# Performance work log

Hardware: AMD Instinct MI355X
Metric: run time of the kernel (lower is better)

## Reference

```python
import jax, jax.numpy as jnp
import numpy as np

NPOINT = 2048  # S after transition-down (init npoint)
NSAMPLE = 16   # K neighbors (init nsample)
EPS = 1e-5     # BatchNorm eps


def _conv1d(w, b, x):  # w [O,I], x [B,I,N] -> [B,O,N]
    y = jnp.einsum('oi,bin->bon', w, x)
    return y if b is None else y + b[None, :, None]


def _conv2d(w, b, x):  # w [O,I], x [B,I,S,K] -> [B,O,S,K]
    y = jnp.einsum('oi,bisk->bosk', w, x)
    return y if b is None else y + b[None, :, None, None]


def _gather(x, idx):  # x [B,C,N], idx [B,S] -> [B,C,S]
    return jax.vmap(lambda xb, ib: xb[:, ib])(x, idx)


def _group(x, idx):  # x [B,C,N], idx [B,S,K] -> [B,C,S,K]
    return jax.vmap(lambda xb, ib: xb[:, ib])(x, idx)


def _fps(xyz_bnc, S):  # farthest point sampling, start at index 0 (deterministic)
    B, N, _ = xyz_bnc.shape
    def body(carry, _):
        dist, far = carry
        centroid = jnp.take_along_axis(xyz_bnc, far[:, None, None], axis=1)  # [B,1,3]
        d = jnp.sum((xyz_bnc - centroid) ** 2, axis=-1)  # [B,N]
        dist = jnp.minimum(dist, d)
        nxt = jnp.argmax(dist, axis=-1).astype(jnp.int32)
        return (dist, nxt), far
    init = (jnp.full((B, N), 1e10, xyz_bnc.dtype), jnp.zeros((B,), jnp.int32))
    _, idxs = jax.lax.scan(body, init, None, length=S)
    return jnp.transpose(idxs)  # [B,S]


def _knn(k, query, pts):  # query [B,S,3], pts [B,N,3] -> idx [B,S,k]
    d2 = (jnp.sum(query ** 2, -1)[..., None] + jnp.sum(pts ** 2, -1)[:, None, :]
          - 2.0 * jnp.einsum('bsc,bnc->bsn', query, pts))
    _, idx = jax.lax.top_k(-d2, k)
    return idx


def _bn(x, gamma, beta):  # training-mode batchnorm over (B, spatial) per channel
    axes = (0,) + tuple(range(2, x.ndim))
    m = jnp.mean(x, axes, keepdims=True)
    v = jnp.var(x, axes, keepdims=True)
    shp = (1, -1) + (1,) * (x.ndim - 2)
    return gamma.reshape(shp) * (x - m) / jnp.sqrt(v + EPS) + beta.reshape(shp)


def _forward(xyz, points, td_w, td_b, td_gamma, td_beta,
             blk_before_w, blk_before_b, blk_qkv_w,
             blk_pos_w1, blk_pos_b1, blk_pos_w2, blk_pos_b2,
             blk_attn_w1, blk_attn_b1, blk_attn_w2, blk_attn_b2,
             blk_after_w, blk_after_b):
    S, K = NPOINT, NSAMPLE
    xyz_t = jnp.transpose(xyz, (0, 2, 1))  # [B,N,3]
    # ---- PointTransformerTransitionDown ----
    fps_idx = _fps(xyz_t, S)                       # [B,S]
    new_xyz = _gather(xyz, fps_idx)                # [B,3,S]
    new_xyz_t = jnp.transpose(new_xyz, (0, 2, 1))  # [B,S,3]
    gidx = _knn(K, new_xyz_t, xyz_t)               # [B,S,K]
    grouped_xyz = _group(xyz, gidx) - new_xyz[:, :, :, None]   # [B,3,S,K]
    grouped = jnp.concatenate([_group(points, gidx), grouped_xyz], axis=1)  # [B,D+3,S,K]
    h = jax.nn.relu(_bn(_conv2d(td_w, td_b, grouped), td_gamma, td_beta))
    pts = jnp.max(h, axis=-1)  # [B,out,S]
    # ---- PointTransformerResBlocks ----
    sgidx = _knn(K, new_xyz_t, new_xyz_t)          # self-KNN [B,S,K]
    gxyz = new_xyz[:, :, :, None] - _group(new_xyz, sgidx)  # [B,3,S,K]
    num_attn = blk_before_w.shape[0]
    for i in range(num_attn):
        rel = _conv2d(blk_pos_w2[i], blk_pos_b2[i],
                      jax.nn.relu(_conv2d(blk_pos_w1[i], blk_pos_b1[i], gxyz)))  # [B,mid,S,K]
        p = _conv1d(blk_before_w[i], blk_before_b[i], pts)   # [B,mid,S]
        qkv = _conv1d(blk_qkv_w[i], None, p)                 # [B,3*mid,S]
        q, k_, v = jnp.split(qkv, 3, axis=1)
        qk_rel = q[:, :, :, None] - _group(k_, sgidx)        # [B,mid,S,K]
        v = _group(v, sgidx) + rel
        sim = _conv2d(blk_attn_w2[i], blk_attn_b2[i],
                      jax.nn.relu(_conv2d(blk_attn_w1[i], blk_attn_b1[i], qk_rel + rel)))
        attn = jax.nn.softmax(sim, axis=-1)                  # softmax over neighbors
        agg = jnp.sum(attn * v, axis=-1)                     # [B,mid,S]
        pts = pts + _conv1d(blk_after_w[i], blk_after_b[i], agg)
    return new_xyz, pts


def setup_inputs() -> dict:
    key = jax.random.key(0)
    ks = jax.random.split(key, 20)
    B, N, Din, Dout, mid, A = 4, 8192, 64, 128, 32, 2
    r = lambda k, s, sc: sc * jax.random.normal(k, s, dtype=jnp.float32)
    return {
        'xyz': r(ks[0], (B, 3, N), 1.0),
        'points': r(ks[1], (B, Din, N), 1.0),
        'td_w': r(ks[2], (Dout, Din + 3), 0.1), 'td_b': r(ks[3], (Dout,), 0.02),
        'td_gamma': jnp.ones((Dout,), jnp.float32), 'td_beta': jnp.zeros((Dout,), jnp.float32),
        'blk_before_w': r(ks[4], (A, mid, Dout), 0.1), 'blk_before_b': r(ks[5], (A, mid), 0.02),
        'blk_qkv_w': r(ks[6], (A, 3 * mid, mid), 0.1),
        'blk_pos_w1': r(ks[7], (A, 64, 3), 0.1), 'blk_pos_b1': r(ks[8], (A, 64), 0.02),
        'blk_pos_w2': r(ks[9], (A, mid, 64), 0.1), 'blk_pos_b2': r(ks[10], (A, mid), 0.02),
        'blk_attn_w1': r(ks[11], (A, 4 * mid, mid), 0.1), 'blk_attn_b1': r(ks[12], (A, 4 * mid), 0.02),
        'blk_attn_w2': r(ks[13], (A, mid, 4 * mid), 0.1), 'blk_attn_b2': r(ks[14], (A, mid), 0.02),
        'blk_after_w': r(ks[15], (A, Dout, mid), 0.1), 'blk_after_b': r(ks[16], (A, Dout), 0.02),
    }


def reference(xyz, points, td_w, td_b, td_gamma, td_beta,
              blk_before_w, blk_before_b, blk_qkv_w,
              blk_pos_w1, blk_pos_b1, blk_pos_w2, blk_pos_b2,
              blk_attn_w1, blk_attn_b1, blk_attn_w2, blk_attn_b2,
              blk_after_w, blk_after_b):
    return _forward(xyz, points, td_w, td_b, td_gamma, td_beta,
                    blk_before_w, blk_before_b, blk_qkv_w,
                    blk_pos_w1, blk_pos_b1, blk_pos_w2, blk_pos_b2,
                    blk_attn_w1, blk_attn_b1, blk_attn_w2, blk_attn_b2,
                    blk_after_w, blk_after_b)
```

## Files before the change

### kernel.cpp

```cpp
#include <hip/hip_runtime.h>

#define BB 4
#define NN 8192
#define SS 2048
#define KK 16

typedef float v2f __attribute__((ext_vector_type(2)));

#define FTH 512
#define FPT (NN/FTH)
#define TRB 256
#define SPB 124
__global__ __launch_bounds__(FTH, 1) void fps_kernel(
    const float* __restrict__ xyz,
    const float* __restrict__ points,
    float* __restrict__ out_newxyz,
    float* __restrict__ nxt,
    float* __restrict__ ptst,
    int* __restrict__ spin_flag)
{
  #pragma clang fp contract(off)
  const int blk = blockIdx.x;
  const int tid = threadIdx.x;
  __shared__ __align__(16) float4 sxyz[NN];
  __shared__ __align__(16) unsigned long long skey[2][8];
  __shared__ int smi[SS];
  __shared__ float sred[8*6];
  __shared__ float tile[32][33];

  if (blk >= BB) {
    if (blk < BB + TRB) {
      if (blk == BB && tid == 0) spin_flag[8] = 0;
      const int x = tid & 31, yy = tid >> 5;
      for (int q = 0; q < 8; ++q) {
        const int tj = (blk - BB)*8 + q;
        const int tn = tj & 255, tc = (tj >> 8) & 1, tb = tj >> 9;
        const int n0 = tn*32, c0 = tc*32;
        __syncthreads();
        tile[yy][x]    = points[(tb*64 + c0+yy)*NN + n0+x];
        tile[yy+16][x] = points[(tb*64 + c0+yy+16)*NN + n0+x];
        __syncthreads();
        ptst[(tb*NN + n0+yy)*64 + c0+x]    = tile[x][yy];
        ptst[(tb*NN + n0+yy+16)*64 + c0+x] = tile[x][yy+16];
      }
      return;
    }
    if (tid >= 64) return;
    const int s0 = atomicAdd(spin_flag, 0);
    float a0 = 1.0f + tid, a1 = 2.0f, a2 = 3.0f, a3 = 4.0f;
    for (int outer = 0; outer < 50000; ++outer) {
      #pragma unroll
      for (int u = 0; u < 256; ++u) {
        a0 = fmaf(a0, 1.0000001f, 1e-7f);
        a1 = fmaf(a1, 0.9999999f, 2e-7f);
        a2 = fmaf(a2, 1.0000002f, 3e-7f);
        a3 = fmaf(a3, 0.9999998f, 4e-7f);
      }
      if (atomicAdd(spin_flag, 0) - s0 >= BB) break;
    }
    asm volatile("" :: "v"(a0), "v"(a1), "v"(a2), "v"(a3));
    return;
  }

  const int b = blk;
  const int wave = tid >> 6;
  const int lane = tid & 63;
  const float* xb = xyz + b*3*NN;

  float tx[FPT], ty[FPT], tz[FPT];
  #pragma unroll
  for (int j = 0; j < FPT; ++j) {
    int i = tid + j*FTH;
    tx[j] = xb[i]; ty[j] = xb[NN+i]; tz[j] = xb[2*NN+i];
  }
  float mnx = tx[0], mxx = tx[0], mny = ty[0], mxy = ty[0], mnz = tz[0], mxz = tz[0];
  #pragma unroll
  for (int j = 1; j < FPT; ++j) {
    mnx = fminf(mnx, tx[j]); mxx = fmaxf(mxx, tx[j]);
    mny = fminf(mny, ty[j]); mxy = fmaxf(mxy, ty[j]);
    mnz = fminf(mnz, tz[j]); mxz = fmaxf(mxz, tz[j]);
  }
  #define WRED(var, OP) { \
    float s_; \
    s_ = __int_as_float(__builtin_amdgcn_update_dpp(0, __float_as_int(var), 0x111, 0xf, 0xf, true)); var = OP(var, s_); \
    s_ = __int_as_float(__builtin_amdgcn_update_dpp(0, __float_as_int(var), 0x112, 0xf, 0xf, true)); var = OP(var, s_); \
    s_ = __int_as_float(__builtin_amdgcn_update_dpp(0, __float_as_int(var), 0x114, 0xf, 0xf, true)); var = OP(var, s_); \
    s_ = __int_as_float(__builtin_amdgcn_update_dpp(0, __float_as_int(var), 0x118, 0xf, 0xf, true)); var = OP(var, s_); \
    s_ = __int_as_float(__builtin_amdgcn_update_dpp(0, __float_as_int(var), 0x142, 0xf, 0xf, true)); var = OP(var, s_); \
    s_ = __int_as_float(__builtin_amdgcn_update_dpp(0, __float_as_int(var), 0x143, 0xf, 0xf, true)); var = OP(var, s_); }
  WRED(mnx, fminf) WRED(mxx, fmaxf) WRED(mny, fminf) WRED(mxy, fmaxf) WRED(mnz, fminf) WRED(mxz, fmaxf)
  #undef WRED
  if (lane == 63) {
    sred[wave*6+0] = mnx; sred[wave*6+1] = mxx; sred[wave*6+2] = mny;
    sred[wave*6+3] = mxy; sred[wave*6+4] = mnz; sred[wave*6+5] = mxz;
  }
  smi[tid] = 0;
  __syncthreads();
  #pragma unroll
  for (int w = 0; w < 8; ++w) {
    mnx = fminf(mnx, sred[w*6+0]); mxx = fmaxf(mxx, sred[w*6+1]);
    mny = fminf(mny, sred[w*6+2]); mxy = fmaxf(mxy, sred[w*6+3]);
    mnz = fminf(mnz, sred[w*6+4]); mxz = fmaxf(mxz, sred[w*6+5]);
  }
  const float scx = 8.0f / (mxx - mnx + 1e-12f);
  const float scy = 8.0f / (mxy - mny + 1e-12f);
  const float scz = 8.0f / (mxz - mnz + 1e-12f);
  int cells[FPT];
  #pragma unroll
  for (int j = 0; j < FPT; ++j) {
    int qx = min(7, (int)((tx[j] - mnx) * scx));
    int qy = min(7, (int)((ty[j] - mny) * scy));
    int qz = min(7, (int)((tz[j] - mnz) * scz));
    int m = (qx&1) | ((qy&1)<<1) | ((qz&1)<<2)
          | ((qx&2)<<2) | ((qy&2)<<3) | ((qz&2)<<4)
          | ((qx&4)<<4) | ((qy&4)<<5) | ((qz&4)<<6);
    cells[j] = m;
    atomicAdd(&smi[m], 1);
  }
  __syncthreads();
  for (int d = 1; d < 512; d <<= 1) {
    int v = smi[tid];
    int a = (tid >= d) ? smi[tid - d] : 0;
    __syncthreads();
    smi[tid] = v + a;
    __syncthreads();
  }
  {
    int excl = (tid == 0) ? 0 : smi[tid - 1];
    smi[512 + tid] = excl;
  }
  __syncthreads();
  #pragma unroll
  for (int j = 0; j < FPT; ++j) {
    int pos = atomicAdd(&smi[512 + cells[j]], 1);
    sxyz[pos] = make_float4(tx[j], ty[j], tz[j], 0.0f);
  }
  __syncthreads();
  v2f px[FPT/2], py[FPT/2], pz[FPT/2], dist[FPT/2];
  float bx0, bx1, by0, by1, bz0, bz1;
  {
    float4 c0 = sxyz[tid*FPT];
    bx0 = bx1 = c0.x; by0 = by1 = c0.y; bz0 = bz1 = c0.z;
    #pragma unroll
    for (int e = 0; e < FPT; ++e) {
      float4 cc = sxyz[tid*FPT + e];
      ((float*)px)[e] = cc.x; ((float*)py)[e] = cc.y; ((float*)pz)[e] = cc.z;
      ((float*)dist)[e] = 1e10f;
      bx0 = fminf(bx0, cc.x); bx1 = fmaxf(bx1, cc.x);
      by0 = fminf(by0, cc.y); by1 = fmaxf(by1, cc.y);
      bz0 = fminf(bz0, cc.z); bz1 = fmaxf(bz1, cc.z);
    }
  }
  float dmax = 1e10f;
  int   beste = 0;
  float cx = xb[0], cy = xb[NN], cz = xb[2*NN];
  __syncthreads();
  for (int it = 1; it < SS; ++it) {
    const int buf = it & 1;
    float gx = fmaxf(fmaxf(bx0 - cx, cx - bx1), 0.0f);
    float gy = fmaxf(fmaxf(by0 - cy, cy - by1), 0.0f);
    float gz = fmaxf(fmaxf(bz0 - cz, cz - bz1), 0.0f);
    float lb = gx*gx + gy*gy; lb = lb + gz*gz;
    if (lb * 0.99999f < dmax) {
      v2f cx2 = {cx, cx}, cy2 = {cy, cy}, cz2 = {cz, cz};
      v2f vmax = {-1.0f, -1.0f};
      #pragma unroll
      for (int j = 0; j < FPT/2; ++j) {
        v2f dx = px[j] - cx2, dy = py[j] - cy2, dz = pz[j] - cz2;
        v2f d = dx*dx + dy*dy;
        d = d + dz*dz;
        v2f nd = __builtin_elementwise_min(dist[j], d);
        dist[j] = nd;
        vmax = __builtin_elementwise_max(vmax, nd);
      }
      float mloc = fmaxf(vmax.x, vmax.y);
      int ce[FPT/2];
      #pragma unroll
      for (int j = 0; j < FPT/2; ++j) {
        int c = 0x7FFFFFFF;
        if (dist[j].y == mloc) c = 2*j + 1;
        if (dist[j].x == mloc) c = 2*j;
        ce[j] = c;
      }
      #pragma unroll
      for (int st = FPT/4; st >= 1; st >>= 1) {
        #pragma unroll
        for (int j = 0; j < st; ++j) ce[j] = ce[j] < ce[j+st] ? ce[j] : ce[j+st];
      }
      dmax = mloc;
      beste = ce[0];
    }
    float wm = dmax;
    #define FPS_MAXR(ctrl) { \
      float s_ = __int_as_float(__builtin_amdgcn_update_dpp(0, __float_as_int(wm), ctrl, 0xf, 0xf, true)); \
      wm = fmaxf(wm, s_); }
    FPS_MAXR(0x111)
    FPS_MAXR(0x112)
    FPS_MAXR(0x114)
    FPS_MAXR(0x118)
    FPS_MAXR(0x142)
    FPS_MAXR(0x143)
    #undef FPS_MAXR
    wm = __int_as_float(__builtin_amdgcn_readlane(__float_as_int(wm), 63));
    unsigned long long em = __ballot(dmax == wm);
    int lw = (int)__ffsll((unsigned long long)em) - 1;
    int bi_w = __builtin_amdgcn_readlane((tid << 4) + beste, lw);
    if (lane == 63) skey[buf][wave] = ((unsigned long long)__float_as_uint(wm) << 32) | (unsigned)~bi_w;
    __syncthreads();
    const ulonglong2* kp = (const ulonglong2*)&skey[buf][0];
    ulonglong2 k01 = kp[0], k23 = kp[1], k45 = kp[2], k67 = kp[3];
    unsigned long long m0 = k01.x > k01.y ? k01.x : k01.y;
    unsigned long long m1 = k23.x > k23.y ? k23.x : k23.y;
    unsigned long long m2 = k45.x > k45.y ? k45.x : k45.y;
    unsigned long long m3 = k67.x > k67.y ? k67.x : k67.y;
    unsigned long long ma = m0 > m1 ? m0 : m1;
    unsigned long long mb = m2 > m3 ? m2 : m3;
    unsigned long long mk = ma > mb ? ma : mb;
    int mi = (int)(~(unsigned)mk);
    float4 c = sxyz[mi];
    if (tid == 0) smi[it] = mi;
    cx = c.x; cy = c.y; cz = c.z;
  }
  __syncthreads();
  for (int it = tid; it < SS; it += FTH) {
    float x, y, z;
    if (it == 0) { x = xb[0]; y = xb[NN]; z = xb[2*NN]; }
    else { float4 c = sxyz[smi[it]]; x = c.x; y = c.y; z = c.z; }
    out_newxyz[(b*3+0)*SS + it] = x;
    out_newxyz[(b*3+1)*SS + it] = y;
    out_newxyz[(b*3+2)*SS + it] = z;
    nxt[(b*SS+it)*3+0] = x; nxt[(b*SS+it)*3+1] = y; nxt[(b*SS+it)*3+2] = z;
  }
  if (tid == 0) atomicAdd(spin_flag, 1);
}

#define TILE 2048
#define KTH 512
__global__ __launch_bounds__(KTH) void knn_kernel(
    const float* __restrict__ query_t,
    const float* __restrict__ cand1,
    const float* __restrict__ cand2,
    int* __restrict__ out1,
    int* __restrict__ out2)
{
  #pragma clang fp contract(off)
  __shared__ float4 sc[TILE];
  __shared__ float  smd[8*64*17];
  __shared__ int    smj[8*64*17];
  const int blocksPerB = SS/64;
  const int half = blockIdx.x >> 7;
  const int blk = blockIdx.x & 127;
  const float* cand = half ? cand2 : cand1;
  const int Nc = half ? SS : NN;
  int* outidx = half ? out2 : out1;
  const int b = blk / blocksPerB;
  const int q0 = (blk % blocksPerB)*64;
  const int wave = threadIdx.x >> 6, lane = threadIdx.x & 63;
  const int s = q0 + lane;
  const float qx = query_t[(b*SS+s)*3+0];
  const float qy = query_t[(b*SS+s)*3+1];
  const float qz = query_t[(b*SS+s)*3+2];
  float sq = qx*qx + qy*qy; sq = sq + qz*qz;
  float d16[16]; int i16[16];
  #pragma unroll
  for (int j = 0; j < 16; ++j) { d16[j] = 1e30f; i16[j] = 0x7FFFFFFF; }
  const float* cb = cand + b*3*Nc;
  const int QL = TILE/8;
  for (int base = 0; base < Nc; base += TILE) {
    __syncthreads();
    for (int j = threadIdx.x; j < TILE; j += KTH) {
      float x = cb[base+j], y = cb[Nc+base+j], z = cb[2*Nc+base+j];
      float pp = x*x + y*y; pp = pp + z*z;
      sc[j] = make_float4(x, y, z, pp);
    }
    __syncthreads();
    const int lo = wave*QL, hi = lo + QL;
    for (int j = lo; j < hi; ++j) {
      float4 c = sc[j];
      float qp = qx*c.x + qy*c.y; qp = qp + qz*c.z;
      float d2 = (sq + c.w) - 2.0f*qp;
      if (d2 < d16[15]) {
        d16[15] = d2; i16[15] = base + j;
        #pragma unroll
        for (int t = 15; t > 0; --t) {
          if (d16[t] < d16[t-1]) {
            float td = d16[t]; d16[t] = d16[t-1]; d16[t-1] = td;
            int   ti = i16[t]; i16[t] = i16[t-1]; i16[t-1] = ti;
          }
        }
      }
    }
  }
  const int off = (wave*64 + lane)*17;
  #pragma unroll
  for (int j = 0; j < 16; ++j) { smd[off+j] = d16[j]; smj[off+j] = i16[j]; }
  __syncthreads();
  if (wave == 0) {
    int p[8] = {0,0,0,0,0,0,0,0};
    for (int o = 0; o < 16; ++o) {
      float bd = 3e38f; int bi = 0x7FFFFFFF, bw = 0;
      #pragma unroll
      for (int w = 0; w < 8; ++w) {
        float d = smd[(w*64+lane)*17 + p[w]];
        int   i = smj[(w*64+lane)*17 + p[w]];
        if (d < bd || (d == bd && i < bi)) { bd = d; bi = i; bw = w; }
      }
      p[bw]++;
      outidx[(b*SS+s)*KK + o] = bi;
    }
  }
}

__global__ __launch_bounds__(128) void td_kernel(
    const float* __restrict__ ptst,
    const float* __restrict__ xyz,
    const float* __restrict__ newxyz,
    const int* __restrict__ gidx,
    const float* __restrict__ td_w,
    const float* __restrict__ td_b,
    float* __restrict__ ymax,
    float* __restrict__ psum,
    float* __restrict__ psq)
{
  const int bs = blockIdx.x;
  const int b = bs >> 11, s = bs & (SS-1);
  const int t = threadIdx.x;
  __shared__ int gi[KK];
  __shared__ float g[67*17];
  if (t < KK) gi[t] = gidx[bs*KK + t];
  __syncthreads();
  #pragma unroll
  for (int base = 0; base < 1024; base += 128) {
    int idx = base + t;
    int i = idx & 63, k = idx >> 6;
    g[i*17 + k] = ptst[(b*NN + gi[k])*64 + i];
  }
  if (t < 48) {
    int c = t >> 4, k = t & 15;
    g[(64+c)*17 + k] = xyz[(b*3+c)*NN + gi[k]] - newxyz[(b*3+c)*SS + s];
  }
  __syncthreads();
  float acc[KK];
  #pragma unroll
  for (int k = 0; k < KK; ++k) acc[k] = 0.0f;
  const float* wrow = td_w + t*67;
  for (int i = 0; i < 67; ++i) {
    float w = wrow[i];
    #pragma unroll
    for (int k = 0; k < KK; ++k) acc[k] = fmaf(w, g[i*17 + k], acc[k]);
  }
  float bias = td_b[t];
  float mx = -1e30f, s1 = 0.f, s2 = 0.f;
  #pragma unroll
  for (int k = 0; k < KK; ++k) {
    float y = acc[k] + bias;
    mx = fmaxf(mx, y);
    s1 += y;
    s2 = fmaf(y, y, s2);
  }
  ymax[bs*128 + t] = mx;
  psum[bs*128 + t] = s1;
  psq [bs*128 + t] = s2;
}

__global__ __launch_bounds__(256) void bn_partial(
    const float* __restrict__ psum, const float* __restrict__ psq,
    float* __restrict__ part1, float* __restrict__ part2,
    const float* __restrict__ gamma, const float* __restrict__ beta,
    float* __restrict__ scale, float* __restrict__ bias,
    int* __restrict__ counter)
{
  const int blk = blockIdx.x, t = threadIdx.x;
  const int c = t & 127, half = t >> 7;
  const float* ps = psum + (blk*64 + half*32)*128;
  const float* pq = psq  + (blk*64 + half*32)*128;
  float s1 = 0.f, s2 = 0.f;
  for (int r = 0; r < 32; ++r) { s1 += ps[r*128 + c]; s2 += pq[r*128 + c]; }
  __shared__ float sh1[256], sh2[256];
  __shared__ int s_last;
  sh1[t] = s1; sh2[t] = s2;
  __syncthreads();
  if (t < 128) {
    part1[blk*128 + t] = sh1[t] + sh1[t+128];
    part2[blk*128 + t] = sh2[t] + sh2[t+128];
  }
  __syncthreads();
  __threadfence();
  if (t == 0) s_last = (atomicAdd(counter, 1) == 127) ? 1 : 0;
  __syncthreads();
  if (!s_last) return;
  __threadfence();
  float f1 = 0.f, f2 = 0.f;
  for (int j = half*64; j < half*64 + 64; ++j) {
    f1 += part1[j*128 + c];
    f2 += part2[j*128 + c];
  }
  sh1[t] = f1; sh2[t] = f2;
  __syncthreads();
  if (t < 128) {
    float a1 = sh1[t] + sh1[t+128];
    float a2 = sh2[t] + sh2[t+128];
    const float n = (float)(BB*SS*KK);
    float mean = a1/n;
    float var  = a2/n - mean*mean;
    float sc = gamma[t] / sqrtf(var + 1e-5f);
    scale[t] = sc;
    bias[t]  = beta[t] - mean*sc;
  }
}

__global__ __launch_bounds__(128) void r1_first(
    const float* __restrict__ ymax,
    const float* __restrict__ scale, const float* __restrict__ bias,
    const float* __restrict__ bw, const float* __restrict__ bb,
    const float* __restrict__ qw,
    float* __restrict__ pts,
    float* __restrict__ qkv)
{
  const int bs = blockIdx.x;
  const int t = threadIdx.x;
  __shared__ float pcol[128];
  __shared__ float p[32];
  float v = fmaxf(fmaf(ymax[bs*128 + t], scale[t], bias[t]), 0.0f);
  pts[bs*128 + t] = v;
  pcol[t] = v;
  __syncthreads();
  if (t < 32) {
    float acc = 0.f;
    const float* w = bw + t*128;
    for (int j = 0; j < 128; ++j) acc = fmaf(w[j], pcol[j], acc);
    p[t] = acc + bb[t];
  }
  __syncthreads();
  if (t < 96) {
    float acc = 0.f;
    const float* w = qw + t*32;
    #pragma unroll
    for (int j = 0; j < 32; ++j) acc = fmaf(w[j], p[j], acc);
    qkv[bs*96 + t] = acc;
  }
}

__global__ __launch_bounds__(128) void r1_kernel(
    const float* __restrict__ pts,
    const float* __restrict__ bw, const float* __restrict__ bb,
    const float* __restrict__ qw,
    float* __restrict__ qkv)
{
  const int bs = blockIdx.x;
  const int t = threadIdx.x;
  __shared__ float pcol[128];
  __shared__ float p[32];
  pcol[t] = pts[bs*128 + t];
  __syncthreads();
  if (t < 32) {
    float acc = 0.f;
    const float* w = bw + t*128;
    for (int j = 0; j < 128; ++j) acc = fmaf(w[j], pcol[j], acc);
    p[t] = acc + bb[t];
  }
  __syncthreads();
  if (t < 96) {
    float acc = 0.f;
    const float* w = qw + t*32;
    #pragma unroll
    for (int j = 0; j < 32; ++j) acc = fmaf(w[j], p[j], acc);
    qkv[bs*96 + t] = acc;
  }
}

__global__ __launch_bounds__(128) void r2_kernel(
    const float* __restrict__ qkv,
    const float* __restrict__ newxyz,
    const int* __restrict__ sgidx,
    const float* __restrict__ pw1, const float* __restrict__ pb1,
    const float* __restrict__ pw2, const float* __restrict__ pb2,
    const float* __restrict__ aw1, const float* __restrict__ ab1,
    const float* __restrict__ aw2, const float* __restrict__ ab2,
    const float* __restrict__ fw,  const float* __restrict__ fb,
    float* __restrict__ pts,
    float* __restrict__ outT)
{
  const int bs = blockIdx.x;
  const int b = bs >> 11, s = bs & (SS-1);
  const int t = threadIdx.x;
  __shared__ int sgi[KK];
  __shared__ float qv[32];
  __shared__ float kn[32*17], vn[32*17];
  __shared__ float gx[3*KK];
  __shared__ float h1[64*KK];
  __shared__ float x2[32*KK];
  __shared__ float a1[128*17];
  __shared__ float simb[32*KK];
  __shared__ float agg[32];
  if (t < KK) sgi[t] = sgidx[bs*KK + t];
  __syncthreads();
  if (t < 32) qv[t] = qkv[bs*96 + t];
  for (int idx = t; idx < 32*KK; idx += 128) {
    int k = idx >> 5, c = idx & 31;
    int base = (b*SS + sgi[k])*96;
    kn[c*17+k] = qkv[base + 32 + c];
    vn[c*17+k] = qkv[base + 64 + c];
  }
  if (t < 3*KK) {
    int c = t >> 4, k = t & 15;
    gx[t] = newxyz[(b*3+c)*SS + s] - newxyz[(b*3+c)*SS + sgi[k]];
  }
  __syncthreads();
  for (int idx = t; idx < 64*KK; idx += 128) {
    int c = idx >> 4, k = idx & 15;
    float acc = 0.f;
    #pragma unroll
    for (int j = 0; j < 3; ++j) acc = fmaf(pw1[c*3+j], gx[j*KK+k], acc);
    h1[idx] = fmaxf(acc + pb1[c], 0.0f);
  }
  __syncthreads();
  for (int idx = t; idx < 32*KK; idx += 128) {
    int c = idx >> 4, k = idx & 15;
    float acc = 0.f;
    const float* w = pw2 + c*64;
    for (int j = 0; j < 64; ++j) acc = fmaf(w[j], h1[j*KK+k], acc);
    float r = acc + pb2[c];
    x2[idx] = (qv[c] - kn[c*17+k]) + r;
    vn[c*17+k] = vn[c*17+k] + r;
  }
  __syncthreads();
  {
    float acc[KK];
    #pragma unroll
    for (int k = 0; k < KK; ++k) acc[k] = 0.f;
    const float* w = aw1 + t*32;
    for (int j = 0; j < 32; ++j) {
      float wv = w[j];
      #pragma unroll
      for (int k = 0; k < KK; ++k) acc[k] = fmaf(wv, x2[j*KK+k], acc[k]);
    }
    float bv = ab1[t];
    #pragma unroll
    for (int k = 0; k < KK; ++k) a1[t*17+k] = fmaxf(acc[k] + bv, 0.0f);
  }
  __syncthreads();
  for (int idx = t; idx < 32*KK; idx += 128) {
    int c = idx >> 4, k = idx & 15;
    float acc = 0.f;
    const float* w = aw2 + c*128;
    for (int j = 0; j < 128; ++j) acc = fmaf(w[j], a1[j*17+k], acc);
    simb[idx] = acc + ab2[c];
  }
  __syncthreads();
  if (t < 32) {
    float m = -1e30f;
    #pragma unroll
    for (int k = 0; k < KK; ++k) m = fmaxf(m, simb[t*KK+k]);
    float sum = 0.f;
    float e[KK];
    #pragma unroll
    for (int k = 0; k < KK; ++k) { e[k] = __expf(simb[t*KK+k] - m); sum += e[k]; }
    float inv = 1.0f / sum;
    float a = 0.f;
    #pragma unroll
    for (int k = 0; k < KK; ++k) a = fmaf(e[k]*inv, vn[t*17+k], a);
    agg[t] = a;
  }
  __syncthreads();
  {
    float acc = 0.f;
    const float* w = fw + t*32;
    #pragma unroll
    for (int j = 0; j < 32; ++j) acc = fmaf(w[j], agg[j], acc);
    float val = pts[bs*128 + t] + (acc + fb[t]);
    if (outT) outT[(b*128 + t)*SS + s] = val;
    else      pts[bs*128 + t] = val;
  }
}

extern "C" void kernel_launch(void* const* d_in, const int* in_sizes, int n_in,
                              void* d_out, int out_size, void* d_ws, size_t ws_size,
                              hipStream_t stream) {
  const float* xyz      = (const float*)d_in[0];
  const float* points   = (const float*)d_in[1];
  const float* td_w     = (const float*)d_in[2];
  const float* td_b     = (const float*)d_in[3];
  const float* td_gamma = (const float*)d_in[4];
  const float* td_beta  = (const float*)d_in[5];
  const float* bw  = (const float*)d_in[6];
  const float* bb  = (const float*)d_in[7];
  const float* qw  = (const float*)d_in[8];
  const float* pw1 = (const float*)d_in[9];
  const float* pb1 = (const float*)d_in[10];
  const float* pw2 = (const float*)d_in[11];
  const float* pb2 = (const float*)d_in[12];
  const float* aw1 = (const float*)d_in[13];
  const float* ab1 = (const float*)d_in[14];
  const float* aw2 = (const float*)d_in[15];
  const float* ab2 = (const float*)d_in[16];
  const float* fw  = (const float*)d_in[17];
  const float* fb  = (const float*)d_in[18];
  float* out = (float*)d_out;
  float* out_newxyz = out;
  float* out_pts    = out + BB*3*SS;

  char* w = (char*)d_ws;
  float* nxt    = (float*)w; w += BB*SS*3*sizeof(float);
  int*   gidx   = (int*)w;   w += BB*SS*KK*sizeof(int);
  int*   sgidx  = (int*)w;   w += BB*SS*KK*sizeof(int);
  float* ymax   = (float*)w; w += BB*128*SS*sizeof(float);
  float* psum   = (float*)w; w += 128*BB*SS*sizeof(float);
  float* psq    = (float*)w; w += 128*BB*SS*sizeof(float);
  float* part1  = (float*)w; w += 128*128*sizeof(float);
  float* part2  = (float*)w; w += 128*128*sizeof(float);
  float* bnscale= (float*)w; w += 256*sizeof(float);
  float* bnbias = (float*)w; w += 256*sizeof(float);
  float* pts    = (float*)w; w += BB*128*SS*sizeof(float);
  float* qkv    = (float*)w; w += BB*96*SS*sizeof(float);
  float* ptst   = (float*)w; w += BB*NN*64*sizeof(float);
  int*   flags  = (int*)w;   w += 256;

  fps_kernel<<<BB + TRB + SPB, FTH, 0, stream>>>(xyz, points, out_newxyz, nxt, ptst, flags);
  knn_kernel<<<2*BB*(SS/64), KTH, 0, stream>>>(nxt, xyz, out_newxyz, gidx, sgidx);
  td_kernel<<<BB*SS, 128, 0, stream>>>(ptst, xyz, out_newxyz, gidx, td_w, td_b, ymax, psum, psq);
  bn_partial<<<128, 256, 0, stream>>>(psum, psq, part1, part2,
      td_gamma, td_beta, bnscale, bnbias, &flags[8]);
  r1_first<<<BB*SS, 128, 0, stream>>>(ymax, bnscale, bnbias, bw, bb, qw, pts, qkv);
  r2_kernel<<<BB*SS, 128, 0, stream>>>(qkv, out_newxyz, sgidx,
      pw1, pb1, pw2, pb2, aw1, ab1, aw2, ab2, fw, fb, pts, nullptr);
  r1_kernel<<<BB*SS, 128, 0, stream>>>(pts, bw + 32*128, bb + 32, qw + 96*32, qkv);
  r2_kernel<<<BB*SS, 128, 0, stream>>>(qkv, out_newxyz, sgidx,
      pw1 + 64*3, pb1 + 64, pw2 + 32*64, pb2 + 32,
      aw1 + 128*32, ab1 + 128, aw2 + 32*128, ab2 + 32,
      fw + 128*32, fb + 128, pts, out_pts);
}
```

Measured before the change: 2.401 ms.

## Prune kNN with Morton-sorted candidate slabs and AABB lower bounds

```diff
diff --git a/kernel.cpp b/kernel.cpp
--- a/kernel.cpp
+++ b/kernel.cpp
@@ -6,6 +6,37 @@
 #define KK 16
 
 typedef float v2f __attribute__((ext_vector_type(2)));
+
+__device__ __forceinline__ float wred_max(float v) {
+  float s;
+  s = __int_as_float(__builtin_amdgcn_update_dpp(0, __float_as_int(v), 0x111, 0xf, 0xf, true)); v = fmaxf(v, s);
+  s = __int_as_float(__builtin_amdgcn_update_dpp(0, __float_as_int(v), 0x112, 0xf, 0xf, true)); v = fmaxf(v, s);
+  s = __int_as_float(__builtin_amdgcn_update_dpp(0, __float_as_int(v), 0x114, 0xf, 0xf, true)); v = fmaxf(v, s);
+  s = __int_as_float(__builtin_amdgcn_update_dpp(0, __float_as_int(v), 0x118, 0xf, 0xf, true)); v = fmaxf(v, s);
+  s = __int_as_float(__builtin_amdgcn_update_dpp(0, __float_as_int(v), 0x142, 0xf, 0xf, true)); v = fmaxf(v, s);
+  s = __int_as_float(__builtin_amdgcn_update_dpp(0, __float_as_int(v), 0x143, 0xf, 0xf, true)); v = fmaxf(v, s);
+  return v;
+}
+__device__ __forceinline__ float wred_min(float v) {
+  float s;
+  s = __int_as_float(__builtin_amdgcn_update_dpp(0, __float_as_int(v), 0x111, 0xf, 0xf, true)); v = fminf(v, s);
+  s = __int_as_float(__builtin_amdgcn_update_dpp(0, __float_as_int(v), 0x112, 0xf, 0xf, true)); v = fminf(v, s);
+  s = __int_as_float(__builtin_amdgcn_update_dpp(0, __float_as_int(v), 0x114, 0xf, 0xf, true)); v = fminf(v, s);
+  s = __int_as_float(__builtin_amdgcn_update_dpp(0, __float_as_int(v), 0x118, 0xf, 0xf, true)); v = fminf(v, s);
+  s = __int_as_float(__builtin_amdgcn_update_dpp(0, __float_as_int(v), 0x142, 0xf, 0xf, true)); v = fminf(v, s);
+  s = __int_as_float(__builtin_amdgcn_update_dpp(0, __float_as_int(v), 0x143, 0xf, 0xf, true)); v = fminf(v, s);
+  return v;
+}
+__device__ __forceinline__ int morton8(float x, float y, float z,
+                                       float mnx, float mny, float mnz,
+                                       float scx, float scy, float scz) {
+  int qx = min(7, (int)((x - mnx) * scx));
+  int qy = min(7, (int)((y - mny) * scy));
+  int qz = min(7, (int)((z - mnz) * scz));
+  return (qx&1) | ((qy&1)<<1) | ((qz&1)<<2)
+       | ((qx&2)<<2) | ((qy&2)<<3) | ((qz&2)<<4)
+       | ((qx&4)<<4) | ((qy&4)<<5) | ((qz&4)<<6);
+}
 
 #define FTH 512
 #define FPT (NN/FTH)
@@ -15,13 +46,18 @@
     const float* __restrict__ xyz,
     const float* __restrict__ points,
     float* __restrict__ out_newxyz,
-    float* __restrict__ nxt,
     float* __restrict__ ptst,
+    float4* __restrict__ csorted,
+    float*  __restrict__ caabb,
+    float4* __restrict__ qsorted,
+    float*  __restrict__ qaabb,
     int* __restrict__ spin_flag)
 {
   #pragma clang fp contract(off)
   const int blk = blockIdx.x;
   const int tid = threadIdx.x;
+  const int wave = tid >> 6;
+  const int lane = tid & 63;
   __shared__ __align__(16) float4 sxyz[NN];
   __shared__ __align__(16) unsigned long long skey[2][8];
   __shared__ int smi[SS];
@@ -43,6 +79,80 @@
         ptst[(tb*NN + n0+yy)*64 + c0+x]    = tile[x][yy];
         ptst[(tb*NN + n0+yy+16)*64 + c0+x] = tile[x][yy+16];
       }
+      if (blk - BB < BB) {
+        const int b2 = blk - BB;
+        const float* xb2 = xyz + b2*3*NN;
+        float tx[FPT], ty[FPT], tz[FPT];
+        #pragma unroll
+        for (int j = 0; j < FPT; ++j) {
+          int i = tid + j*FTH;
+          tx[j] = xb2[i]; ty[j] = xb2[NN+i]; tz[j] = xb2[2*NN+i];
+        }
+        float mnx = tx[0], mxx = tx[0], mny = ty[0], mxy = ty[0], mnz = tz[0], mxz = tz[0];
+        #pragma unroll
+        for (int j = 1; j < FPT; ++j) {
+          mnx = fminf(mnx, tx[j]); mxx = fmaxf(mxx, tx[j]);
+          mny = fminf(mny, ty[j]); mxy = fmaxf(mxy, ty[j]);
+          mnz = fminf(mnz, tz[j]); mxz = fmaxf(mxz, tz[j]);
+        }
+        mnx = wred_min(mnx); mxx = wred_max(mxx);
+        mny = wred_min(mny); mxy = wred_max(mxy);
+        mnz = wred_min(mnz); mxz = wred_max(mxz);
+        if (lane == 63) {
+          sred[wave*6+0] = mnx; sred[wave*6+1] = mxx; sred[wave*6+2] = mny;
+          sred[wave*6+3] = mxy; sred[wave*6+4] = mnz; sred[wave*6+5] = mxz;
+        }
+        smi[tid] = 0;
+        __syncthreads();
+        #pragma unroll
+        for (int w = 0; w < 8; ++w) {
+          mnx = fminf(mnx, sred[w*6+0]); mxx = fmaxf(mxx, sred[w*6+1]);
+          mny = fminf(mny, sred[w*6+2]); mxy = fmaxf(mxy, sred[w*6+3]);
+          mnz = fminf(mnz, sred[w*6+4]); mxz = fmaxf(mxz, sred[w*6+5]);
+        }
+        const float scx = 8.0f / (mxx - mnx + 1e-12f);
+        const float scy = 8.0f / (mxy - mny + 1e-12f);
+        const float scz = 8.0f / (mxz - mnz + 1e-12f);
+        int cells[FPT];
+        #pragma unroll
+        for (int j = 0; j < FPT; ++j) {
+          cells[j] = morton8(tx[j], ty[j], tz[j], mnx, mny, mnz, scx, scy, scz);
+          atomicAdd(&smi[cells[j]], 1);
+        }
+        __syncthreads();
+        for (int d = 1; d < 512; d <<= 1) {
+          int v = smi[tid];
+          int a = (tid >= d) ? smi[tid - d] : 0;
+          __syncthreads();
+          smi[tid] = v + a;
+          __syncthreads();
+        }
+        { int excl = (tid == 0) ? 0 : smi[tid - 1]; smi[512 + tid] = excl; }
+        __syncthreads();
+        #pragma unroll
+        for (int j = 0; j < FPT; ++j) {
+          int pos = atomicAdd(&smi[512 + cells[j]], 1);
+          csorted[b2*NN + pos] = make_float4(tx[j], ty[j], tz[j], __int_as_float(tid + j*FTH));
+        }
+        __syncthreads();
+        for (int sl = wave; sl < 32; sl += 8) {
+          float a0x=1e30f, a1x=-1e30f, a0y=1e30f, a1y=-1e30f, a0z=1e30f, a1z=-1e30f;
+          #pragma unroll
+          for (int t = 0; t < 4; ++t) {
+            float4 c = csorted[b2*NN + sl*256 + lane*4 + t];
+            a0x = fminf(a0x, c.x); a1x = fmaxf(a1x, c.x);
+            a0y = fminf(a0y, c.y); a1y = fmaxf(a1y, c.y);
+            a0z = fminf(a0z, c.z); a1z = fmaxf(a1z, c.z);
+          }
+          a0x = wred_min(a0x); a1x = wred_max(a1x);
+          a0y = wred_min(a0y); a1y = wred_max(a1y);
+          a0z = wred_min(a0z); a1z = wred_max(a1z);
+          if (lane == 63) {
+            float* o = caabb + (b2*32 + sl)*8;
+            o[0]=a0x; o[1]=a1x; o[2]=a0y; o[3]=a1y; o[4]=a0z; o[5]=a1z;
+          }
+        }
+      }
       return;
     }
     if (tid >= 64) return;
@@ -63,8 +173,6 @@
   }
 
   const int b = blk;
-  const int wave = tid >> 6;
-  const int lane = tid & 63;
   const float* xb = xyz + b*3*NN;
 
   float tx[FPT], ty[FPT], tz[FPT];
@@ -80,16 +188,9 @@
     mny = fminf(mny, ty[j]); mxy = fmaxf(mxy, ty[j]);
     mnz = fminf(mnz, tz[j]); mxz = fmaxf(mxz, tz[j]);
   }
-  #define WRED(var, OP) { \
-    float s_; \
-    s_ = __int_as_float(__builtin_amdgcn_update_dpp(0, __float_as_int(var), 0x111, 0xf, 0xf, true)); var = OP(var, s_); \
-    s_ = __int_as_float(__builtin_amdgcn_update_dpp(0, __float_as_int(var), 0x112, 0xf, 0xf, true)); var = OP(var, s_); \
-    s_ = __int_as_float(__builtin_amdgcn_update_dpp(0, __float_as_int(var), 0x114, 0xf, 0xf, true)); var = OP(var, s_); \
-    s_ = __int_as_float(__builtin_amdgcn_update_dpp(0, __float_as_int(var), 0x118, 0xf, 0xf, true)); var = OP(var, s_); \
-    s_ = __int_as_float(__builtin_amdgcn_update_dpp(0, __float_as_int(var), 0x142, 0xf, 0xf, true)); var = OP(var, s_); \
-    s_ = __int_as_float(__builtin_amdgcn_update_dpp(0, __float_as_int(var), 0x143, 0xf, 0xf, true)); var = OP(var, s_); }
-  WRED(mnx, fminf) WRED(mxx, fmaxf) WRED(mny, fminf) WRED(mxy, fmaxf) WRED(mnz, fminf) WRED(mxz, fmaxf)
-  #undef WRED
+  mnx = wred_min(mnx); mxx = wred_max(mxx);
+  mny = wred_min(mny); mxy = wred_max(mxy);
+  mnz = wred_min(mnz); mxz = wred_max(mxz);
   if (lane == 63) {
     sred[wave*6+0] = mnx; sred[wave*6+1] = mxx; sred[wave*6+2] = mny;
     sred[wave*6+3] = mxy; sred[wave*6+4] = mnz; sred[wave*6+5] = mxz;
@@ -108,14 +209,8 @@
   int cells[FPT];
   #pragma unroll
   for (int j = 0; j < FPT; ++j) {
-    int qx = min(7, (int)((tx[j] - mnx) * scx));
-    int qy = min(7, (int)((ty[j] - mny) * scy));
-    int qz = min(7, (int)((tz[j] - mnz) * scz));
-    int m = (qx&1) | ((qy&1)<<1) | ((qz&1)<<2)
-          | ((qx&2)<<2) | ((qy&2)<<3) | ((qz&2)<<4)
-          | ((qx&4)<<4) | ((qy&4)<<5) | ((qz&4)<<6);
-    cells[j] = m;
-    atomicAdd(&smi[m], 1);
+    cells[j] = morton8(tx[j], ty[j], tz[j], mnx, mny, mnz, scx, scy, scz);
+    atomicAdd(&smi[cells[j]], 1);
   }
   __syncthreads();
   for (int d = 1; d < 512; d <<= 1) {
@@ -191,16 +286,7 @@
       beste = ce[0];
     }
     float wm = dmax;
-    #define FPS_MAXR(ctrl) { \
-      float s_ = __int_as_float(__builtin_amdgcn_update_dpp(0, __float_as_int(wm), ctrl, 0xf, 0xf, true)); \
-      wm = fmaxf(wm, s_); }
-    FPS_MAXR(0x111)
-    FPS_MAXR(0x112)
-    FPS_MAXR(0x114)
-    FPS_MAXR(0x118)
-    FPS_MAXR(0x142)
-    FPS_MAXR(0x143)
-    #undef FPS_MAXR
+    wm = wred_max(wm);
     wm = __int_as_float(__builtin_amdgcn_readlane(__float_as_int(wm), 63));
     unsigned long long em = __ballot(dmax == wm);
     int lw = (int)__ffsll((unsigned long long)em) - 1;
@@ -229,86 +315,129 @@
     out_newxyz[(b*3+0)*SS + it] = x;
     out_newxyz[(b*3+1)*SS + it] = y;
     out_newxyz[(b*3+2)*SS + it] = z;
-    nxt[(b*SS+it)*3+0] = x; nxt[(b*SS+it)*3+1] = y; nxt[(b*SS+it)*3+2] = z;
+  }
+  float4 qp4[4]; int qj4[4], qc4[4];
+  #pragma unroll
+  for (int k2 = 0; k2 < 4; ++k2) {
+    int j = tid + k2*FTH;
+    float4 p;
+    if (j == 0) p = make_float4(xb[0], xb[NN], xb[2*NN], 0.0f);
+    else        p = sxyz[smi[j]];
+    qp4[k2] = p; qj4[k2] = j;
+  }
+  __syncthreads();
+  smi[tid] = 0;
+  __syncthreads();
+  #pragma unroll
+  for (int k2 = 0; k2 < 4; ++k2) {
+    qc4[k2] = morton8(qp4[k2].x, qp4[k2].y, qp4[k2].z, mnx, mny, mnz, scx, scy, scz);
+    atomicAdd(&smi[qc4[k2]], 1);
+  }
+  __syncthreads();
+  for (int d = 1; d < 512; d <<= 1) {
+    int v = smi[tid];
+    int a = (tid >= d) ? smi[tid - d] : 0;
+    __syncthreads();
+    smi[tid] = v + a;
+    __syncthreads();
+  }
+  { int excl = (tid == 0) ? 0 : smi[tid - 1]; smi[512 + tid] = excl; }
+  __syncthreads();
+  #pragma unroll
+  for (int k2 = 0; k2 < 4; ++k2) {
+    int pos = atomicAdd(&smi[512 + qc4[k2]], 1);
+    qsorted[b*SS + pos] = make_float4(qp4[k2].x, qp4[k2].y, qp4[k2].z, __int_as_float(qj4[k2]));
+  }
+  __syncthreads();
+  {
+    float a0x=1e30f, a1x=-1e30f, a0y=1e30f, a1y=-1e30f, a0z=1e30f, a1z=-1e30f;
+    #pragma unroll
+    for (int t = 0; t < 4; ++t) {
+      float4 c = qsorted[b*SS + wave*256 + lane*4 + t];
+      a0x = fminf(a0x, c.x); a1x = fmaxf(a1x, c.x);
+      a0y = fminf(a0y, c.y); a1y = fmaxf(a1y, c.y);
+      a0z = fminf(a0z, c.z); a1z = fmaxf(a1z, c.z);
+    }
+    a0x = wred_min(a0x); a1x = wred_max(a1x);
+    a0y = wred_min(a0y); a1y = wred_max(a1y);
+    a0z = wred_min(a0z); a1z = wred_max(a1z);
+    if (lane == 63) {
+      float* o = qaabb + (b*8 + wave)*8;
+      o[0]=a0x; o[1]=a1x; o[2]=a0y; o[3]=a1y; o[4]=a0z; o[5]=a1z;
+    }
   }
   if (tid == 0) atomicAdd(spin_flag, 1);
 }
 
-#define TILE 2048
-#define KTH 512
-__global__ __launch_bounds__(KTH) void knn_kernel(
-    const float* __restrict__ query_t,
-    const float* __restrict__ cand1,
-    const float* __restrict__ cand2,
+__global__ __launch_bounds__(64) void knn_kernel(
+    const float4* __restrict__ qsorted,
+    const float*  __restrict__ qaabb,
+    const float4* __restrict__ csorted,
+    const float*  __restrict__ caabb,
     int* __restrict__ out1,
     int* __restrict__ out2)
 {
   #pragma clang fp contract(off)
-  __shared__ float4 sc[TILE];
-  __shared__ float  smd[8*64*17];
-  __shared__ int    smj[8*64*17];
-  const int blocksPerB = SS/64;
-  const int half = blockIdx.x >> 7;
-  const int blk = blockIdx.x & 127;
-  const float* cand = half ? cand2 : cand1;
-  const int Nc = half ? SS : NN;
+  __shared__ float4 sc[256];
+  __shared__ int    sidx[256];
+  const int bid = blockIdx.x;
+  const int half = bid >> 7;
+  const int rem = bid & 127;
+  const int b = rem >> 5;
+  const int wslot = rem & 31;
+  const int lane = threadIdx.x;
+  const float4* cand = half ? (qsorted + b*SS) : (csorted + b*NN);
+  const float*  aabb = half ? (qaabb + b*8*8) : (caabb + b*32*8);
+  const int nsl = half ? 8 : 32;
+  const int s0 = half ? (wslot >> 2) : wslot;
   int* outidx = half ? out2 : out1;
-  const int b = blk / blocksPerB;
-  const int q0 = (blk % blocksPerB)*64;
-  const int wave = threadIdx.x >> 6, lane = threadIdx.x & 63;
-  const int s = q0 + lane;
-  const float qx = query_t[(b*SS+s)*3+0];
-  const float qy = query_t[(b*SS+s)*3+1];
-  const float qz = query_t[(b*SS+s)*3+2];
+
+  float4 q = qsorted[b*SS + wslot*64 + lane];
+  const int orig_s = __float_as_int(q.w);
+  const float qx = q.x, qy = q.y, qz = q.z;
   float sq = qx*qx + qy*qy; sq = sq + qz*qz;
   float d16[16]; int i16[16];
   #pragma unroll
   for (int j = 0; j < 16; ++j) { d16[j] = 1e30f; i16[j] = 0x7FFFFFFF; }
-  const float* cb = cand + b*3*Nc;
-  const int QL = TILE/8;
-  for (int base = 0; base < Nc; base += TILE) {
+
+  for (int j = 0; j < nsl; ++j) {
+    int off = (j + 1) >> 1;
+    int s = (s0 + ((j & 1) ? off : -off)) & (nsl - 1);
+    const float* ab = aabb + s*8;
+    float gx = fmaxf(fmaxf(ab[0] - qx, qx - ab[1]), 0.0f);
+    float gy = fmaxf(fmaxf(ab[2] - qy, qy - ab[3]), 0.0f);
+    float gz = fmaxf(fmaxf(ab[4] - qz, qz - ab[5]), 0.0f);
+    float lbnd = gx*gx + gy*gy; lbnd = lbnd + gz*gz;
+    bool skip = (lbnd * 0.9999f - 1e-3f) > d16[15];
+    if (__all(skip)) continue;
+    #pragma unroll
+    for (int t = 0; t < 4; ++t) {
+      float4 c = cand[s*256 + t*64 + lane];
+      float pp = c.x*c.x + c.y*c.y; pp = pp + c.z*c.z;
+      sidx[t*64 + lane] = __float_as_int(c.w);
+      sc[t*64 + lane] = make_float4(c.x, c.y, c.z, pp);
+    }
     __syncthreads();
-    for (int j = threadIdx.x; j < TILE; j += KTH) {
-      float x = cb[base+j], y = cb[Nc+base+j], z = cb[2*Nc+base+j];
-      float pp = x*x + y*y; pp = pp + z*z;
-      sc[j] = make_float4(x, y, z, pp);
-    }
-    __syncthreads();
-    const int lo = wave*QL, hi = lo + QL;
-    for (int j = lo; j < hi; ++j) {
-      float4 c = sc[j];
+    for (int t = 0; t < 256; ++t) {
+      float4 c = sc[t];
       float qp = qx*c.x + qy*c.y; qp = qp + qz*c.z;
       float d2 = (sq + c.w) - 2.0f*qp;
       if (d2 < d16[15]) {
-        d16[15] = d2; i16[15] = base + j;
+        d16[15] = d2; i16[15] = sidx[t];
         #pragma unroll
-        for (int t = 15; t > 0; --t) {
-          if (d16[t] < d16[t-1]) {
-            float td = d16[t]; d16[t] = d16[t-1]; d16[t-1] = td;
-            int   ti = i16[t]; i16[t] = i16[t-1]; i16[t-1] = ti;
+        for (int u = 15; u > 0; --u) {
+          if (d16[u] < d16[u-1]) {
+            float td = d16[u]; d16[u] = d16[u-1]; d16[u-1] = td;
+            int   ti = i16[u]; i16[u] = i16[u-1]; i16[u-1] = ti;
           }
         }
       }
     }
-  }
-  const int off = (wave*64 + lane)*17;
-  #pragma unroll
-  for (int j = 0; j < 16; ++j) { smd[off+j] = d16[j]; smj[off+j] = i16[j]; }
-  __syncthreads();
-  if (wave == 0) {
-    int p[8] = {0,0,0,0,0,0,0,0};
-    for (int o = 0; o < 16; ++o) {
-      float bd = 3e38f; int bi = 0x7FFFFFFF, bw = 0;
-      #pragma unroll
-      for (int w = 0; w < 8; ++w) {
-        float d = smd[(w*64+lane)*17 + p[w]];
-        int   i = smj[(w*64+lane)*17 + p[w]];
-        if (d < bd || (d == bd && i < bi)) { bd = d; bi = i; bw = w; }
-      }
-      p[bw]++;
-      outidx[(b*SS+s)*KK + o] = bi;
-    }
-  }
+    __syncthreads();
+  }
+  #pragma unroll
+  for (int o = 0; o < 16; ++o)
+    outidx[(b*SS + orig_s)*KK + o] = i16[o];
 }
 
 __global__ __launch_bounds__(128) void td_kernel(
@@ -601,7 +730,6 @@
   float* out_pts    = out + BB*3*SS;
 
   char* w = (char*)d_ws;
-  float* nxt    = (float*)w; w += BB*SS*3*sizeof(float);
   int*   gidx   = (int*)w;   w += BB*SS*KK*sizeof(int);
   int*   sgidx  = (int*)w;   w += BB*SS*KK*sizeof(int);
   float* ymax   = (float*)w; w += BB*128*SS*sizeof(float);
@@ -615,9 +743,14 @@
   float* qkv    = (float*)w; w += BB*96*SS*sizeof(float);
   float* ptst   = (float*)w; w += BB*NN*64*sizeof(float);
   int*   flags  = (int*)w;   w += 256;
-
-  fps_kernel<<<BB + TRB + SPB, FTH, 0, stream>>>(xyz, points, out_newxyz, nxt, ptst, flags);
-  knn_kernel<<<2*BB*(SS/64), KTH, 0, stream>>>(nxt, xyz, out_newxyz, gidx, sgidx);
+  float4* csorted = (float4*)w; w += BB*NN*sizeof(float4);
+  float*  caabb   = (float*)w;  w += BB*32*8*sizeof(float);
+  float4* qsorted = (float4*)w; w += BB*SS*sizeof(float4);
+  float*  qaabb   = (float*)w;  w += BB*8*8*sizeof(float);
+
+  fps_kernel<<<BB + TRB + SPB, FTH, 0, stream>>>(xyz, points, out_newxyz, ptst,
+      csorted, caabb, qsorted, qaabb, flags);
+  knn_kernel<<<256, 64, 0, stream>>>(qsorted, qaabb, csorted, caabb, gidx, sgidx);
   td_kernel<<<BB*SS, 128, 0, stream>>>(ptst, xyz, out_newxyz, gidx, td_w, td_b, ymax, psum, psq);
   bn_partial<<<128, 256, 0, stream>>>(psum, psq, part1, part2,
       td_gamma, td_beta, bnscale, bnbias, &flags[8]);
```

After: 2.876 ms. 19.8% more time.
